# Kernel optimization log

Measured on AMD Instinct MI355X. Metric: run time of the kernel, lower is better.

## Reference

```python
import jax, jax.numpy as jnp
import numpy as np
from jax import lax

NEG = -1e9  # matches torch masked_fill value


def cyk(s, lens):
    """Inside algorithm (logsumexp semiring) over closed spans.

    s: [B, N, N] span log-potentials, s[b,i,j] scores span covering tokens i..j (inclusive).
    lens: [B] int sentence lengths. Returns log partition alpha[b, 0, lens[b]-1].
    """
    B, N, _ = s.shape
    ar = jnp.arange(N)
    # width-1 spans on the diagonal
    alpha = jnp.full((B, N, N), NEG, s.dtype).at[:, ar, ar].set(s[:, ar, ar])
    i2 = jnp.broadcast_to(ar[:, None], (N, N))  # start index i
    u2 = jnp.broadcast_to(ar[None, :], (N, N))  # split offset: left width u+1

    def step(alpha, w):
        j = ar + w - 1                           # end index per start, [N]
        jc = jnp.clip(j, 0, N - 1)
        li = jnp.clip(i2 + u2, 0, N - 1)         # left span end i+u
        ri = jnp.clip(i2 + u2 + 1, 0, N - 1)     # right span start i+u+1
        left = alpha[:, i2, li]                  # [B,N,N] alpha[b, i, i+u]
        right = alpha[:, ri, jnp.broadcast_to(jc[:, None], (N, N))]  # alpha[b, i+u+1, j]
        valid = (u2 <= w - 2) & (j[:, None] < N)
        comb = jnp.where(valid[None], left + right, NEG)
        new = jax.nn.logsumexp(comb, axis=-1) + s[:, ar, jc]  # [B,N]
        old = alpha[:, ar, jc]
        new = jnp.where((j < N)[None], new, old)
        return alpha.at[:, ar, jc].set(new), None

    alpha, _ = lax.scan(jax.checkpoint(step), alpha, jnp.arange(2, N + 1))
    return alpha[jnp.arange(B), 0, lens - 1]


def setup_inputs() -> dict:
    key = jax.random.key(0)
    k1, k2, k3 = jax.random.split(key, 3)
    B, N = 16, 256
    lens = jax.random.randint(k1, (B,), N // 2, N + 1)
    pos = jnp.arange(N)
    tok = pos[None, :] < lens[:, None]                 # [B,N] token mask
    maskspan = tok[:, None, :] & tok[:, :, None]       # [B,N,N]
    upper = pos[None, :] >= pos[:, None]               # j >= i
    valid_span = maskspan & upper[None]
    span_mask = ~valid_span                            # True = invalid span
    spans_ind = (jax.random.uniform(k2, (B, N, N)) < 0.05) & valid_span  # gold spans
    span_logits = jax.random.normal(k3, (B, N, N, 2), jnp.float32)
    return {"span_logits": span_logits, "spans_ind": spans_ind,
            "maskspan": maskspan, "span_mask": span_mask}


def reference(span_logits, spans_ind, maskspan, span_mask):
    spans_ind = spans_ind.astype(bool)
    # observed (constrained) potentials: smoothing == 1.0 branch
    ch0 = jnp.where(span_mask | spans_ind, NEG, span_logits[..., 0])
    ch1 = jnp.where(span_mask | ~spans_ind, NEG, span_logits[..., 1])
    ob = jnp.logaddexp(ch0, ch1)                       # [B,N,N]
    allp = jax.nn.logsumexp(span_logits, axis=-1)      # [B,N,N]
    lens = maskspan[:, 0].sum(-1)                      # [B]
    marginals = cyk(ob, lens)
    logz = cyk(allp, lens)
    loss_spans = (logz - marginals).sum() / maskspan[:, 0].sum()
    return loss_spans
```

## Files before the change

kernel.cpp:

```cpp
#include <hip/hip_runtime.h>
#include <hip/hip_bf16.h>
#include <cstdint>
#include <cstddef>

#define NTHREADS 1024
#define NWAVES 16
#define BB 16
#define NN 256
#define EPAD_TOTAL 33280
#define PSTRIDE 68

typedef unsigned char u8;

__device__ __forceinline__ bool mask_val(const void* p, size_t idx, bool isbyte) {
  return isbyte ? (((const u8*)p)[idx] != 0) : (((const int*)p)[idx] != 0);
}

__device__ __forceinline__ float score_val(float2 v, const void* sind, size_t cell,
                                           int run, bool isbyte) {
  if (run == 0) return mask_val(sind, cell, isbyte) ? v.y : v.x;
  float m = fmaxf(v.x, v.y);
  return m + __logf(1.f + __expf(-fabsf(v.x - v.y)));
}

__device__ __forceinline__ int Fpad(int M) {
  int f = M >> 2, r = M & 3;
  return 8*f*f + 8*f + 4*r*(f+1);
}

extern "C" __global__ void __launch_bounds__(NTHREADS, 1)
cyk_kernel(const float2* __restrict__ slog, const void* __restrict__ sind,
           const void* __restrict__ mspan, float* __restrict__ wsv) {
  __shared__ __align__(16) float E[EPAD_TOTAL];
  __shared__ __align__(16) float4 ft4[NN];
  __shared__ float Mar[NN];
  __shared__ unsigned RmaxU[NN];
  __shared__ int off4[NN + 1];
  __shared__ float Part[NWAVES * PSTRIDE];
  __shared__ float scratch[NWAVES];

  const int b = blockIdx.x >> 1;
  const int run = blockIdx.x & 1;
  const int tid = threadIdx.x;
  const int lane = tid & 63;
  const int q = tid >> 6;
  const bool isbyte = ((const u8*)mspan)[1] != 0;
  const size_t sbase = (size_t)b * (NN * NN);

  int pred = 0;
  if (tid < NN) pred = mask_val(mspan, sbase + tid, isbyte) ? 1 : 0;
  const int len = __syncthreads_count(pred);

  if (tid <= NN) off4[tid] = Fpad(NN) - Fpad(NN - tid);
  for (int k = tid; k < EPAD_TOTAL; k += NTHREADS) E[k] = 0.f;
  if (tid < NN) RmaxU[tid] = 0u;
  __syncthreads();

  float a0 = -3.0e38f;
  if (tid < len) {
    size_t cell = sbase + (size_t)tid * NN + tid;
    a0 = score_val(slog[cell], sind, cell, run, isbyte);
  }
  float wm = a0;
  #pragma unroll
  for (int o = 1; o < 64; o <<= 1) wm = fmaxf(wm, __shfl_xor(wm, o, 64));
  if (lane == 0) scratch[q] = wm;
  __syncthreads();
  float M0 = scratch[0];
  #pragma unroll
  for (int k = 1; k < NWAVES; ++k) M0 = fmaxf(M0, scratch[k]);
  if (tid < len) E[tid] = __expf(a0 - M0);
  if (tid == 0) { Mar[0] = M0; RmaxU[0] = __float_as_uint(1.0f); }
  double MarD = (double)M0;
  __syncthreads();

  float myScore = 0.f;

  for (int w = 2; w <= len; ++w) {
    const int S = w - 1;
    const int Cw = len - w + 1;

    if (tid >= 768) {
      const int u = tid - 768;
      if (u < S) {
        const int vd = S - 1 - u;
        const float Gw = Mar[w - 2] + Mar[0];
        double ex = (double)Mar[u] + (double)Mar[vd] - (double)Gw;
        float4 t;
        t.x = __expf((float)ex);
        t.y = __int_as_float(off4[u]);
        t.z = __int_as_float(off4[vd] + u + 1);
        t.w = 0.f;
        ft4[u] = t;
      }
    } else if (w > 2) {
      const int Cp = len - w + 2;
      if (q < ((Cp + 63) >> 6)) {
        const int c = (q << 6) + lane;
        const int WCGp = (Cp <= 64) ? 1 : (Cp <= 128 ? 2 : 4);
        const int WUp = NWAVES / WCGp;
        float mx = 0.f;
        if (c < Cp) {
          float s = 0.f;
          const int base = (c >> 6) * WUp * PSTRIDE + (c & 63);
          for (int k = 0; k < WUp; ++k) s += Part[base + k * PSTRIDE];
          const int dp = w - 2;
          const float corr = (Mar[w - 3] + Mar[0]) - Mar[dp];
          const float V = s * __expf(myScore + corr);
          E[off4[dp] + c] = V;
          mx = V;
        }
        #pragma unroll
        for (int o = 1; o < 64; o <<= 1) mx = fmaxf(mx, __shfl_xor(mx, o, 64));
        if (lane == 0) atomicMax(&RmaxU[w - 2], __float_as_uint(mx));
      }
    }
    __syncthreads();

    {
      const int WCG = (Cw <= 64) ? 1 : (Cw <= 128 ? 2 : 4);
      const int lw = (WCG == 1) ? 4 : (WCG == 2) ? 3 : 2;
      const int WU = 1 << lw;
      const int cg = q >> lw;
      const int us = q & (WU - 1);
      const int c = (cg << 6) + lane;
      if (c < Cw) {
        float s = 0.f;
        #pragma unroll 4
        for (int u = us; u < S; u += WU) {
          const float4 t = ft4[u];
          s = fmaf(t.x * E[__float_as_int(t.y) + c], E[__float_as_int(t.z) + c], s);
        }
        Part[q * PSTRIDE + (c & 63)] = s;
      }
      if (q < ((Cw + 63) >> 6)) {
        const int cf = (q << 6) + lane;
        if (cf < Cw) {
          const size_t cell = sbase + (size_t)cf * NN + (cf + (w - 1));
          myScore = score_val(slog[cell], sind, cell, run, isbyte);
        }
      }
      if (tid == 0) {
        float lr = __logf(__uint_as_float(RmaxU[w - 2] | 1u));
        lr = fminf(fmaxf(lr, -40.f), 40.f);
        MarD += (double)lr;
        Mar[w - 1] = (float)MarD;
      }
    }
    __syncthreads();
  }

  if (tid == 0) {
    float ssum = 0.f;
    for (int k = 0; k < NWAVES; ++k) ssum += Part[k * PSTRIDE + 0];
    const float corr = (Mar[len - 2] + Mar[0]) - Mar[len - 1];
    double alpha = (double)Mar[len - 1] + (double)(myScore + corr) + (double)__logf(ssum);
    wsv[run * BB + b] = (float)alpha;
    if (run == 0) wsv[2 * BB + b] = (float)len;
  }
}

extern "C" __global__ void loss_kernel(const float* __restrict__ wsv, float* __restrict__ out) {
  const int t = threadIdx.x;
  float diff = 0.0f, ln = 0.0f;
  if (t < BB) { diff = wsv[BB + t] - wsv[t]; ln = wsv[2 * BB + t]; }
  #pragma unroll
  for (int o = 1; o < 64; o <<= 1) {
    diff += __shfl_xor(diff, o, 64);
    ln += __shfl_xor(ln, o, 64);
  }
  if (t == 0) out[0] = diff / ln;
}

extern "C" void kernel_launch(void* const* d_in, const int* in_sizes, int n_in,
                              void* d_out, int out_size, void* d_ws, size_t ws_size,
                              hipStream_t stream) {
  const float2* slog = (const float2*)d_in[0];
  const void* sind = d_in[1];
  const void* mspan = d_in[2];
  float* wsv = (float*)d_ws;
  cyk_kernel<<<dim3(BB * 2), dim3(NTHREADS), 0, stream>>>(slog, sind, mspan, wsv);
  loss_kernel<<<dim3(1), dim3(64), 0, stream>>>(wsv, (float*)d_out);
}
```

Before: 626.9 us.

## Register-block CYK split loop with per-thread column vectors and strided split partition

Restructures the inner split-sum so each wave owns a strided subset of split points and each lane computes 2 or 4 adjacent columns, using vector LDS loads for the left operand and incrementally computed addresses instead of per-split offset tables. The per-split factors are stored transposed so each wave reads four of them with one vector load, and the reduction over partial sums now runs over a flat column index. The aim is fewer LDS instructions per FMA and less address arithmetic. The cost is more register pressure, and waves work on unequal numbers of splits, which can leave load imbalance when widths are small.

```diff
diff --git a/kernel.cpp b/kernel.cpp
--- a/kernel.cpp
+++ b/kernel.cpp
@@ -4,11 +4,10 @@
 #include <cstddef>
 
 #define NTHREADS 1024
-#define NWAVES 16
 #define BB 16
 #define NN 256
-#define EPAD_TOTAL 33280
-#define PSTRIDE 68
+#define EPAD 33792
+#define PSTR 260
 
 typedef unsigned char u8;
 
@@ -31,13 +30,13 @@
 extern "C" __global__ void __launch_bounds__(NTHREADS, 1)
 cyk_kernel(const float2* __restrict__ slog, const void* __restrict__ sind,
            const void* __restrict__ mspan, float* __restrict__ wsv) {
-  __shared__ __align__(16) float E[EPAD_TOTAL];
-  __shared__ __align__(16) float4 ft4[NN];
+  __shared__ __align__(16) float E[EPAD];
+  __shared__ __align__(16) float fp[NN];
   __shared__ float Mar[NN];
   __shared__ unsigned RmaxU[NN];
   __shared__ int off4[NN + 1];
-  __shared__ float Part[NWAVES * PSTRIDE];
-  __shared__ float scratch[NWAVES];
+  __shared__ __align__(16) float Part[16 * PSTR];
+  __shared__ float scratch[16];
 
   const int b = blockIdx.x >> 1;
   const int run = blockIdx.x & 1;
@@ -51,8 +50,9 @@
   if (tid < NN) pred = mask_val(mspan, sbase + tid, isbyte) ? 1 : 0;
   const int len = __syncthreads_count(pred);
 
-  if (tid <= NN) off4[tid] = Fpad(NN) - Fpad(NN - tid);
-  for (int k = tid; k < EPAD_TOTAL; k += NTHREADS) E[k] = 0.f;
+  if (tid <= NN) off4[tid] = 33280 - Fpad(NN - tid);
+  for (int k = tid; k < EPAD; k += NTHREADS) E[k] = 0.f;
+  for (int k = tid; k < 16 * PSTR; k += NTHREADS) Part[k] = 0.f;
   if (tid < NN) RmaxU[tid] = 0u;
   __syncthreads();
 
@@ -68,7 +68,7 @@
   __syncthreads();
   float M0 = scratch[0];
   #pragma unroll
-  for (int k = 1; k < NWAVES; ++k) M0 = fmaxf(M0, scratch[k]);
+  for (int k = 1; k < 16; ++k) M0 = fmaxf(M0, scratch[k]);
   if (tid < len) E[tid] = __expf(a0 - M0);
   if (tid == 0) { Mar[0] = M0; RmaxU[0] = __float_as_uint(1.0f); }
   double MarD = (double)M0;
@@ -82,63 +82,99 @@
 
     if (tid >= 768) {
       const int u = tid - 768;
+      float f = 0.f;
       if (u < S) {
         const int vd = S - 1 - u;
-        const float Gw = Mar[w - 2] + Mar[0];
-        double ex = (double)Mar[u] + (double)Mar[vd] - (double)Gw;
-        float4 t;
-        t.x = __expf((float)ex);
-        t.y = __int_as_float(off4[u]);
-        t.z = __int_as_float(off4[vd] + u + 1);
-        t.w = 0.f;
-        ft4[u] = t;
-      }
+        double ex = (double)Mar[u] + (double)Mar[vd]
+                  - (double)(Mar[w - 2] + Mar[0]);
+        f = __expf((float)ex);
+      }
+      fp[((u & 15) << 4) + (u >> 4)] = f;
     } else if (w > 2) {
-      const int Cp = len - w + 2;
-      if (q < ((Cp + 63) >> 6)) {
-        const int c = (q << 6) + lane;
-        const int WCGp = (Cp <= 64) ? 1 : (Cp <= 128 ? 2 : 4);
-        const int WUp = NWAVES / WCGp;
-        float mx = 0.f;
-        if (c < Cp) {
-          float s = 0.f;
-          const int base = (c >> 6) * WUp * PSTRIDE + (c & 63);
-          for (int k = 0; k < WUp; ++k) s += Part[base + k * PSTRIDE];
-          const int dp = w - 2;
-          const float corr = (Mar[w - 3] + Mar[0]) - Mar[dp];
-          const float V = s * __expf(myScore + corr);
-          E[off4[dp] + c] = V;
-          mx = V;
-        }
+      const int Cp = Cw + 1;
+      const int c = tid;
+      float mx = 0.f;
+      if (c < Cp) {
+        float s = 0.f;
         #pragma unroll
-        for (int o = 1; o < 64; o <<= 1) mx = fmaxf(mx, __shfl_xor(mx, o, 64));
-        if (lane == 0) atomicMax(&RmaxU[w - 2], __float_as_uint(mx));
-      }
+        for (int k = 0; k < 16; ++k) s += Part[k * PSTR + c];
+        const float corr = (Mar[w - 3] + Mar[0]) - Mar[w - 2];
+        const float V = s * __expf(myScore + corr);
+        E[off4[w - 2] + c] = V;
+        mx = V;
+      }
+      #pragma unroll
+      for (int o = 1; o < 64; o <<= 1) mx = fmaxf(mx, __shfl_xor(mx, o, 64));
+      if (lane == 0 && mx > 0.f) atomicMax(&RmaxU[w - 2], __float_as_uint(mx));
     }
     __syncthreads();
 
     {
-      const int WCG = (Cw <= 64) ? 1 : (Cw <= 128 ? 2 : 4);
-      const int lw = (WCG == 1) ? 4 : (WCG == 2) ? 3 : 2;
-      const int WU = 1 << lw;
-      const int cg = q >> lw;
-      const int us = q & (WU - 1);
-      const int c = (cg << 6) + lane;
-      if (c < Cw) {
-        float s = 0.f;
-        #pragma unroll 4
-        for (int u = us; u < S; u += WU) {
-          const float4 t = ft4[u];
-          s = fmaf(t.x * E[__float_as_int(t.y) + c], E[__float_as_int(t.z) + c], s);
+      const int us = q;
+      const int nj = (us < S) ? ((S - us + 15) >> 4) : 0;
+      const int fbase = us << 4;
+
+      if (Cw > 128) {
+        const int c0 = lane << 2;
+        float s0 = 0.f, s1 = 0.f, s2 = 0.f, s3 = 0.f;
+        if (nj > 0) {
+          const int vd0 = S - 1 - us;
+          int aL = off4[us] + c0;
+          int aR = off4[vd0] + us + 1 + c0;
+          int dL = 4000 - 16 * us;
+          int dR = 16 * vd0 - 4240;
+          #define ITER4(FV)                                                \
+            { const float4 L = *(const float4*)&E[aL];                     \
+              const float r0 = E[aR], r1 = E[aR+1], r2 = E[aR+2], r3 = E[aR+3]; \
+              s0 = fmaf((FV) * L.x, r0, s0);                               \
+              s1 = fmaf((FV) * L.y, r1, s1);                               \
+              s2 = fmaf((FV) * L.z, r2, s2);                               \
+              s3 = fmaf((FV) * L.w, r3, s3);                               \
+              aL += dL; dL -= 256; aR += dR; dR -= 256; }
+          const int nj4 = nj >> 2;
+          for (int j4 = 0; j4 < nj4; ++j4) {
+            const float4 ff = *(const float4*)&fp[fbase + (j4 << 2)];
+            ITER4(ff.x) ITER4(ff.y) ITER4(ff.z) ITER4(ff.w)
+          }
+          for (int t = nj & ~3; t < nj; ++t) {
+            const float f1 = fp[fbase + t];
+            ITER4(f1)
+          }
+          #undef ITER4
         }
-        Part[q * PSTRIDE + (c & 63)] = s;
-      }
-      if (q < ((Cw + 63) >> 6)) {
-        const int cf = (q << 6) + lane;
-        if (cf < Cw) {
-          const size_t cell = sbase + (size_t)cf * NN + (cf + (w - 1));
-          myScore = score_val(slog[cell], sind, cell, run, isbyte);
+        *(float4*)&Part[q * PSTR + c0] = make_float4(s0, s1, s2, s3);
+      } else {
+        const int c0 = lane << 1;
+        float s0 = 0.f, s1 = 0.f;
+        if (nj > 0) {
+          const int vd0 = S - 1 - us;
+          int aL = off4[us] + c0;
+          int aR = off4[vd0] + us + 1 + c0;
+          int dL = 4000 - 16 * us;
+          int dR = 16 * vd0 - 4240;
+          #define ITER2(FV)                                                \
+            { const float2 L = *(const float2*)&E[aL];                     \
+              const float r0 = E[aR], r1 = E[aR+1];                        \
+              s0 = fmaf((FV) * L.x, r0, s0);                               \
+              s1 = fmaf((FV) * L.y, r1, s1);                               \
+              aL += dL; dL -= 256; aR += dR; dR -= 256; }
+          const int nj4 = nj >> 2;
+          for (int j4 = 0; j4 < nj4; ++j4) {
+            const float4 ff = *(const float4*)&fp[fbase + (j4 << 2)];
+            ITER2(ff.x) ITER2(ff.y) ITER2(ff.z) ITER2(ff.w)
+          }
+          for (int t = nj & ~3; t < nj; ++t) {
+            const float f1 = fp[fbase + t];
+            ITER2(f1)
+          }
+          #undef ITER2
         }
+        *(float2*)&Part[q * PSTR + c0] = make_float2(s0, s1);
+      }
+
+      if (tid < Cw) {
+        const size_t cell = sbase + (size_t)tid * NN + (tid + w - 1);
+        myScore = score_val(slog[cell], sind, cell, run, isbyte);
       }
       if (tid == 0) {
         float lr = __logf(__uint_as_float(RmaxU[w - 2] | 1u));
@@ -152,9 +188,11 @@
 
   if (tid == 0) {
     float ssum = 0.f;
-    for (int k = 0; k < NWAVES; ++k) ssum += Part[k * PSTRIDE + 0];
+    #pragma unroll
+    for (int k = 0; k < 16; ++k) ssum += Part[k * PSTR];
     const float corr = (Mar[len - 2] + Mar[0]) - Mar[len - 1];
-    double alpha = (double)Mar[len - 1] + (double)(myScore + corr) + (double)__logf(ssum);
+    double alpha = (double)Mar[len - 1] + (double)(myScore + corr)
+                 + (double)__logf(ssum);
     wsv[run * BB + b] = (float)alpha;
     if (run == 0) wsv[2 * BB + b] = (float)len;
   }
```

Result: slower. 673.4 us (+7.4%).

## Store inside scores in bf16 with aligned per-diagonal layout and vectorized split loop

Applied to the files above, without the earlier changes.

Rewrites the CYK inner loop so that exponentiated inside scores live in shared memory as bf16, with separate left and right copies. Each diagonal is padded so that every thread can load four adjacent cells in one 64-bit read. Each wave handles a strided set of split points and picks its split factors by readlane from a transposed table. Partial sums are also kept in bf16, and widths 2 and 3 get a special case. The goal is to cut LDS traffic and per-split address work, at the cost of bf16 rounding error accumulating through the recursion.

```diff
diff --git a/kernel.cpp b/kernel.cpp
--- a/kernel.cpp
+++ b/kernel.cpp
@@ -1,158 +1,242 @@
 #include <hip/hip_runtime.h>
-#include <hip/hip_bf16.h>
 #include <cstdint>
 #include <cstddef>
 
-#define NTHREADS 1024
-#define NWAVES 16
+#define NTH 1024
 #define BB 16
 #define NN 256
-#define EPAD_TOTAL 33280
-#define PSTRIDE 68
+#define ELSZ 34560
+#define PARTSZ 4608
 
 typedef unsigned char u8;
-
-__device__ __forceinline__ bool mask_val(const void* p, size_t idx, bool isbyte) {
-  return isbyte ? (((const u8*)p)[idx] != 0) : (((const int*)p)[idx] != 0);
-}
-
-__device__ __forceinline__ float score_val(float2 v, const void* sind, size_t cell,
-                                           int run, bool isbyte) {
-  if (run == 0) return mask_val(sind, cell, isbyte) ? v.y : v.x;
+typedef unsigned short u16;
+typedef unsigned int u32;
+
+__device__ __forceinline__ bool mask_val(const void* p, size_t i, bool isb) {
+  return isb ? (((const u8*)p)[i] != 0) : (((const int*)p)[i] != 0);
+}
+__device__ __forceinline__ float score_val(float2 v, const void* sind, size_t cell, int run, bool isb) {
+  if (run == 0) return mask_val(sind, cell, isb) ? v.y : v.x;
   float m = fmaxf(v.x, v.y);
   return m + __logf(1.f + __expf(-fabsf(v.x - v.y)));
 }
-
-__device__ __forceinline__ int Fpad(int M) {
-  int f = M >> 2, r = M & 3;
-  return 8*f*f + 8*f + 4*r*(f+1);
-}
-
-extern "C" __global__ void __launch_bounds__(NTHREADS, 1)
+__device__ __forceinline__ u16 f2bf(float x) {
+  u32 u = __float_as_uint(x);
+  return (u16)((u + 0x7fffu + ((u >> 16) & 1u)) >> 16);
+}
+__device__ __forceinline__ float bf2f(u16 h) { return __uint_as_float(((u32)h) << 16); }
+
+template <int P>
+__device__ __forceinline__ void inner_u(
+    const u16* __restrict__ ELu, const u16* __restrict__ ERu, u16* __restrict__ PartU,
+    const float* __restrict__ fp, const int* __restrict__ BLs, const int* __restrict__ BRs,
+    int S, int q, int lane) {
+  constexpr int NL = 64 / P;
+  constexpr int h = 16 * P;
+  constexpr int h2 = h * h;
+  constexpr int RST = (P == 1) ? 260 : (P == 2) ? 132 : 68;
+  const int s4 = q & 3;
+  const int g = lane / NL;
+  const int r = lane % NL;
+  const int c0 = 4 * r - s4;
+  const int nk = (q < S) ? ((S - q + 15) >> 4) : 0;
+  const int nj = (nk + P - 1) / P;
+  const int fb0 = __float_as_int(fp[q * 17 + (lane & 15)]);
+  const int u0 = q + 16 * g;
+  const int v0 = S - 1 - u0;
+  const int v0c = v0 < 0 ? 0 : v0;
+  const int vhc = (v0 - h) < 0 ? 0 : (v0 - h);
+  int aL = BLs[u0] + c0;
+  int dL = BLs[u0 + h] - BLs[u0];
+  int aR = BRs[v0c] + u0 + 1 + c0;
+  int dR = BRs[vhc] - BRs[v0c] + h;
+  float s0 = 0.f, s1 = 0.f, s2 = 0.f, s3 = 0.f;
+  #pragma unroll 4
+  for (int j = 0; j < nj; ++j) {
+    float f;
+    if (P == 1) {
+      f = __int_as_float(__builtin_amdgcn_readlane(fb0, j));
+    } else if (P == 2) {
+      const float fa = __int_as_float(__builtin_amdgcn_readlane(fb0, 2 * j));
+      const float fb = __int_as_float(__builtin_amdgcn_readlane(fb0, 2 * j + 1));
+      f = g ? fb : fa;
+    } else {
+      const float fa = __int_as_float(__builtin_amdgcn_readlane(fb0, 4 * j));
+      const float fb = __int_as_float(__builtin_amdgcn_readlane(fb0, 4 * j + 1));
+      const float fc = __int_as_float(__builtin_amdgcn_readlane(fb0, 4 * j + 2));
+      const float fd = __int_as_float(__builtin_amdgcn_readlane(fb0, 4 * j + 3));
+      f = (g & 2) ? ((g & 1) ? fd : fc) : ((g & 1) ? fb : fa);
+    }
+    const bool val = (j * P + g) < nk;
+    const int aLr = val ? aL : 0;
+    const int aRr = val ? aR : 0;
+    const uint2 Lw = *(const uint2*)(ELu + aLr);
+    const uint2 Rw = *(const uint2*)(ERu + aRr);
+    const float l0 = __uint_as_float(Lw.x << 16);
+    const float l1 = __uint_as_float(Lw.x & 0xffff0000u);
+    const float l2 = __uint_as_float(Lw.y << 16);
+    const float l3 = __uint_as_float(Lw.y & 0xffff0000u);
+    const float r0 = __uint_as_float(Rw.x << 16);
+    const float r1 = __uint_as_float(Rw.x & 0xffff0000u);
+    const float r2 = __uint_as_float(Rw.y << 16);
+    const float r3 = __uint_as_float(Rw.y & 0xffff0000u);
+    s0 = fmaf(f * l0, r0, s0);
+    s1 = fmaf(f * l1, r1, s1);
+    s2 = fmaf(f * l2, r2, s2);
+    s3 = fmaf(f * l3, r3, s3);
+    aL += dL; dL -= h2;
+    aR += dR; dR -= h2;
+  }
+  const int row = q * P + g;
+  const u32 p0 = (u32)f2bf(s0) | ((u32)f2bf(s1) << 16);
+  const u32 p1 = (u32)f2bf(s2) | ((u32)f2bf(s3) << 16);
+  *(uint2*)(PartU + row * RST + (s4 + c0)) = make_uint2(p0, p1);
+}
+
+extern "C" __global__ void __launch_bounds__(NTH, 1)
 cyk_kernel(const float2* __restrict__ slog, const void* __restrict__ sind,
            const void* __restrict__ mspan, float* __restrict__ wsv) {
-  __shared__ __align__(16) float E[EPAD_TOTAL];
-  __shared__ __align__(16) float4 ft4[NN];
+  __shared__ __align__(16) u16 ELu[ELSZ];
+  __shared__ __align__(16) u16 ERu[ELSZ];
+  __shared__ __align__(16) u16 PartU[PARTSZ];
+  __shared__ float fp[272];
   __shared__ float Mar[NN];
-  __shared__ unsigned RmaxU[NN];
-  __shared__ int off4[NN + 1];
-  __shared__ float Part[NWAVES * PSTRIDE];
-  __shared__ float scratch[NWAVES];
+  __shared__ u32 RmaxU[NN];
+  __shared__ int BLs[260];
+  __shared__ int BRs[260];
+  __shared__ float scr[16];
 
   const int b = blockIdx.x >> 1;
   const int run = blockIdx.x & 1;
   const int tid = threadIdx.x;
   const int lane = tid & 63;
   const int q = tid >> 6;
-  const bool isbyte = ((const u8*)mspan)[1] != 0;
+  const bool isb = ((const u8*)mspan)[1] != 0;
   const size_t sbase = (size_t)b * (NN * NN);
 
   int pred = 0;
-  if (tid < NN) pred = mask_val(mspan, sbase + tid, isbyte) ? 1 : 0;
+  if (tid < NN) pred = mask_val(mspan, sbase + tid, isb) ? 1 : 0;
   const int len = __syncthreads_count(pred);
 
-  if (tid <= NN) off4[tid] = Fpad(NN) - Fpad(NN - tid);
-  for (int k = tid; k < EPAD_TOTAL; k += NTHREADS) E[k] = 0.f;
+  if (tid == 0) {
+    BLs[0] = 4; BRs[0] = 7;
+    for (int d = 0; d < 259; ++d) {
+      int sz = len - d; if (sz < 0) sz = 0;
+      int nl_ = BLs[d] + sz;
+      BLs[d + 1] = nl_ + 4 + ((((d + 1 - nl_) % 4) + 4) % 4);
+      int nr_ = BRs[d] + sz;
+      BRs[d + 1] = nr_ + 4 + ((((3 - nr_) % 4) + 4) % 4);
+    }
+  } else {
+    for (int k = tid - 1; k < ELSZ / 2; k += NTH - 1) ((u32*)ELu)[k] = 0u;
+    for (int k = tid - 1; k < ELSZ / 2; k += NTH - 1) ((u32*)ERu)[k] = 0u;
+  }
   if (tid < NN) RmaxU[tid] = 0u;
   __syncthreads();
 
   float a0 = -3.0e38f;
   if (tid < len) {
     size_t cell = sbase + (size_t)tid * NN + tid;
-    a0 = score_val(slog[cell], sind, cell, run, isbyte);
+    a0 = score_val(slog[cell], sind, cell, run, isb);
   }
   float wm = a0;
   #pragma unroll
   for (int o = 1; o < 64; o <<= 1) wm = fmaxf(wm, __shfl_xor(wm, o, 64));
-  if (lane == 0) scratch[q] = wm;
+  if (lane == 0) scr[q] = wm;
   __syncthreads();
-  float M0 = scratch[0];
+  float M0 = scr[0];
   #pragma unroll
-  for (int k = 1; k < NWAVES; ++k) M0 = fmaxf(M0, scratch[k]);
-  if (tid < len) E[tid] = __expf(a0 - M0);
+  for (int k = 1; k < 16; ++k) M0 = fmaxf(M0, scr[k]);
+  if (tid < len) {
+    u16 e0 = f2bf(__expf(a0 - M0));
+    ELu[BLs[0] + tid] = e0;
+    ERu[BRs[0] + tid] = e0;
+  }
   if (tid == 0) { Mar[0] = M0; RmaxU[0] = __float_as_uint(1.0f); }
   double MarD = (double)M0;
   __syncthreads();
 
   float myScore = 0.f;
+  int prevRows = 1, prevRST = 260, prevLgP = 0;
 
   for (int w = 2; w <= len; ++w) {
     const int S = w - 1;
-    const int Cw = len - w + 1;
+    const int C = len - w + 1;
 
     if (tid >= 768) {
-      const int u = tid - 768;
-      if (u < S) {
-        const int vd = S - 1 - u;
-        const float Gw = Mar[w - 2] + Mar[0];
-        double ex = (double)Mar[u] + (double)Mar[vd] - (double)Gw;
-        float4 t;
-        t.x = __expf((float)ex);
-        t.y = __int_as_float(off4[u]);
-        t.z = __int_as_float(off4[vd] + u + 1);
-        t.w = 0.f;
-        ft4[u] = t;
-      }
-    } else if (w > 2) {
+      if (w >= 4) {
+        const int u = tid - 768;
+        float fv = 0.f;
+        if (u < S) {
+          const int vd = S - 1 - u;
+          double ex = (double)Mar[u] + (double)Mar[vd] - (double)Mar[w - 2] - (double)Mar[0];
+          float exf = fminf((float)ex, 80.f);
+          fv = __expf(exf);
+        }
+        fp[(u & 15) * 17 + (u >> 4)] = fv;
+      }
+    } else if (w >= 3) {
+      const int c = tid;
       const int Cp = len - w + 2;
-      if (q < ((Cp + 63) >> 6)) {
-        const int c = (q << 6) + lane;
-        const int WCGp = (Cp <= 64) ? 1 : (Cp <= 128 ? 2 : 4);
-        const int WUp = NWAVES / WCGp;
-        float mx = 0.f;
-        if (c < Cp) {
-          float s = 0.f;
-          const int base = (c >> 6) * WUp * PSTRIDE + (c & 63);
-          for (int k = 0; k < WUp; ++k) s += Part[base + k * PSTRIDE];
-          const int dp = w - 2;
-          const float corr = (Mar[w - 3] + Mar[0]) - Mar[dp];
-          const float V = s * __expf(myScore + corr);
-          E[off4[dp] + c] = V;
-          mx = V;
+      float mx = 0.f;
+      if (c < Cp) {
+        float acc = 0.f;
+        for (int k = 0; k < prevRows; ++k)
+          acc += bf2f(PartU[k * prevRST + (((k >> prevLgP) & 3) + c)]);
+        const float corr = (Mar[w - 3] + Mar[0]) - Mar[w - 2];
+        const float V = acc * __expf(myScore + corr);
+        const u16 vb = f2bf(V);
+        ELu[BLs[w - 2] + c] = vb;
+        ERu[BRs[w - 2] + c] = vb;
+        mx = V;
+      }
+      #pragma unroll
+      for (int o = 1; o < 64; o <<= 1) mx = fmaxf(mx, __shfl_xor(mx, o, 64));
+      if (lane == 0 && mx > 0.f) atomicMax(&RmaxU[w - 2], __float_as_uint(mx));
+    }
+    __syncthreads();
+
+    if (w <= 3) {
+      float sa = 0.f;
+      if (tid < C) {
+        if (w == 2) {
+          sa = bf2f(ELu[BLs[0] + tid]) * bf2f(ELu[BLs[0] + tid + 1]);
+        } else {
+          sa = bf2f(ELu[BLs[0] + tid]) * bf2f(ELu[BLs[1] + tid + 1])
+             + bf2f(ELu[BLs[1] + tid]) * bf2f(ELu[BLs[0] + tid + 2]);
         }
-        #pragma unroll
-        for (int o = 1; o < 64; o <<= 1) mx = fmaxf(mx, __shfl_xor(mx, o, 64));
-        if (lane == 0) atomicMax(&RmaxU[w - 2], __float_as_uint(mx));
-      }
-    }
-    __syncthreads();
-
-    {
-      const int WCG = (Cw <= 64) ? 1 : (Cw <= 128 ? 2 : 4);
-      const int lw = (WCG == 1) ? 4 : (WCG == 2) ? 3 : 2;
-      const int WU = 1 << lw;
-      const int cg = q >> lw;
-      const int us = q & (WU - 1);
-      const int c = (cg << 6) + lane;
-      if (c < Cw) {
-        float s = 0.f;
-        #pragma unroll 4
-        for (int u = us; u < S; u += WU) {
-          const float4 t = ft4[u];
-          s = fmaf(t.x * E[__float_as_int(t.y) + c], E[__float_as_int(t.z) + c], s);
-        }
-        Part[q * PSTRIDE + (c & 63)] = s;
-      }
-      if (q < ((Cw + 63) >> 6)) {
-        const int cf = (q << 6) + lane;
-        if (cf < Cw) {
-          const size_t cell = sbase + (size_t)cf * NN + (cf + (w - 1));
-          myScore = score_val(slog[cell], sind, cell, run, isbyte);
-        }
-      }
-      if (tid == 0) {
-        float lr = __logf(__uint_as_float(RmaxU[w - 2] | 1u));
-        lr = fminf(fmaxf(lr, -40.f), 40.f);
-        MarD += (double)lr;
-        Mar[w - 1] = (float)MarD;
-      }
+        PartU[tid] = f2bf(sa);
+      }
+      prevRows = 1; prevRST = 260; prevLgP = 0;
+    } else {
+      if (C + 3 > 128) {
+        inner_u<1>(ELu, ERu, PartU, fp, BLs, BRs, S, q, lane);
+        prevRows = 16; prevRST = 260; prevLgP = 0;
+      } else if (C + 3 > 64) {
+        inner_u<2>(ELu, ERu, PartU, fp, BLs, BRs, S, q, lane);
+        prevRows = 32; prevRST = 132; prevLgP = 1;
+      } else {
+        inner_u<4>(ELu, ERu, PartU, fp, BLs, BRs, S, q, lane);
+        prevRows = 64; prevRST = 68; prevLgP = 2;
+      }
+    }
+    if (tid < C) {
+      const size_t cell = sbase + (size_t)tid * NN + (tid + w - 1);
+      myScore = score_val(slog[cell], sind, cell, run, isb);
+    }
+    if (tid == 0) {
+      float lr = __logf(__uint_as_float(RmaxU[w - 2] | 1u));
+      lr = fminf(fmaxf(lr, -40.f), 40.f);
+      MarD += (double)lr;
+      Mar[w - 1] = (float)MarD;
     }
     __syncthreads();
   }
 
   if (tid == 0) {
     float ssum = 0.f;
-    for (int k = 0; k < NWAVES; ++k) ssum += Part[k * PSTRIDE + 0];
+    for (int k = 0; k < prevRows; ++k)
+      ssum += bf2f(PartU[k * prevRST + ((k >> prevLgP) & 3)]);
     const float corr = (Mar[len - 2] + Mar[0]) - Mar[len - 1];
     double alpha = (double)Mar[len - 1] + (double)(myScore + corr) + (double)__logf(ssum);
     wsv[run * BB + b] = (float)alpha;
@@ -179,6 +263,6 @@
   const void* sind = d_in[1];
   const void* mspan = d_in[2];
   float* wsv = (float*)d_ws;
-  cyk_kernel<<<dim3(BB * 2), dim3(NTHREADS), 0, stream>>>(slog, sind, mspan, wsv);
+  cyk_kernel<<<dim3(BB * 2), dim3(NTH), 0, stream>>>(slog, sind, mspan, wsv);
   loss_kernel<<<dim3(1), dim3(64), 0, stream>>>(wsv, (float*)d_out);
 }
```

After: 665.9 us. 6.2% more time.
